# Kernel optimization log

Hardware: AMD Instinct MI355X
Metric: run time of the kernel (lower is better)

Reference implementation:

```python
import jax, jax.numpy as jnp
import numpy as np

N_NODES = 100000
N_EDGES = 1000000
NODE_DIM = 128
LR_VOCAB = 2000
LR_EMBED = 32
HIDDEN = 128
IN_DIM = NODE_DIM * 4 + 1 + LR_EMBED  # 545


def setup_inputs() -> dict:
    key = jax.random.key(0)
    ks = jax.random.split(key, 10)
    z = jax.random.normal(ks[0], (N_NODES, NODE_DIM), dtype=jnp.float32)
    edge_index = jax.random.randint(ks[1], (2, N_EDGES), 0, N_NODES, dtype=jnp.int64)
    # edge_attr7: col 0 = dist (float in [0,1)), col 2 = lr_id (int-valued float in [0, LR_VOCAB))
    ea = jax.random.uniform(ks[2], (N_EDGES, 7), dtype=jnp.float32)
    lr_ids = jax.random.randint(ks[3], (N_EDGES,), 0, LR_VOCAB).astype(jnp.float32)
    edge_attr7 = ea.at[:, 2].set(lr_ids)
    lr_emb = jax.random.normal(ks[4], (LR_VOCAB, LR_EMBED), dtype=jnp.float32) * 0.02
    W1 = jax.random.normal(ks[5], (IN_DIM, HIDDEN), dtype=jnp.float32) * 0.02
    b1 = jnp.zeros((HIDDEN,), dtype=jnp.float32)
    W2 = jax.random.normal(ks[6], (HIDDEN, HIDDEN), dtype=jnp.float32) * 0.02
    b2 = jnp.zeros((HIDDEN,), dtype=jnp.float32)
    W3 = jax.random.normal(ks[7], (HIDDEN, 1), dtype=jnp.float32) * 0.02
    b3 = jnp.zeros((1,), dtype=jnp.float32)
    return {"z": z, "edge_index": edge_index, "edge_attr7": edge_attr7,
            "lr_emb": lr_emb, "W1": W1, "b1": b1, "W2": W2, "b2": b2,
            "W3": W3, "b3": b3}


def reference(z, edge_index, edge_attr7, lr_emb, W1, b1, W2, b2, W3, b3):
    src = edge_index[0]
    dst = edge_index[1]
    zs = z[src]                      # [E, D]
    zd = z[dst]                      # [E, D]
    dist = edge_attr7[:, 0:1]        # [E, 1]
    lr_id = edge_attr7[:, 2].astype(jnp.int32)
    lr_vec = lr_emb[lr_id]           # [E, LR_EMBED]
    x = jnp.concatenate([zs, zd, zs * zd, jnp.abs(zs - zd), dist, lr_vec], axis=1)  # [E, IN_DIM]
    h = jax.nn.relu(x @ W1 + b1)     # dropout is identity at inference
    h = jax.nn.relu(h @ W2 + b2)
    logit = (h @ W3 + b3).reshape(-1)  # [E]
    return logit
```

## Files before the change

kernel.cpp:

```cpp
#include <hip/hip_runtime.h>

#define N_EDGES 1000000
#define HID 128
#define ME 64

typedef unsigned short ushort;
typedef unsigned int uint;
typedef __attribute__((ext_vector_type(8))) short short8;
typedef __attribute__((ext_vector_type(4))) float f32x4;

__device__ __forceinline__ float blo(uint u) { return __builtin_bit_cast(float, u << 16); }
__device__ __forceinline__ float bhi(uint u) { return __builtin_bit_cast(float, u & 0xffff0000u); }
__device__ __forceinline__ ushort f2bfbits(float f) {
  uint u = __builtin_bit_cast(uint, f);
  return (ushort)((u + 0x7fffu + ((u >> 16) & 1u)) >> 16);
}
__device__ __forceinline__ uint cvtpk(float a, float b) {
  uint r;
  asm("v_cvt_pk_bf16_f32 %0, %1, %2" : "=v"(r) : "v"(a), "v"(b));
  return r;
}
__device__ __forceinline__ uint cvtpk_abs(float a, float b) {
  uint r;
  asm("v_cvt_pk_bf16_f32 %0, abs(%1), abs(%2)" : "=v"(r) : "v"(a), "v"(b));
  return r;
}
__device__ __forceinline__ int sidx(int r, int c) {
  return r * 128 + (c ^ ((r & 7) << 3));
}

__global__ void prep_kernel(const float* __restrict__ W1, const float* __restrict__ W2,
                            ushort* __restrict__ W1p, ushort* __restrict__ W2p) {
  const int t = blockIdx.x * blockDim.x + threadIdx.x;
  const int n1 = 18 * 8 * 64 * 8;
  if (t < n1) {
    const int j = t & 7, lane = (t >> 3) & 63, nt = (t >> 9) & 7, kb = t >> 12;
    const int col = nt * 16 + (lane & 15);
    float val = 0.f;
    if (kb < 16) {
      const int k = kb * 32 + (lane >> 4) * 8 + j;
      val = W1[k * HID + col];
    } else {
      const int c = (kb - 16) * 32 + (lane >> 4) * 8 + j;
      const int k = (c == 0) ? 512 : ((c >= 2 && c < 34) ? (511 + c) : -1);
      if (k >= 0) val = W1[k * HID + col];
    }
    W1p[t] = f2bfbits(val);
  } else {
    const int t2 = t - n1;
    if (t2 < 4 * 8 * 64 * 8) {
      const int j = t2 & 7, lane = (t2 >> 3) & 63, nt = (t2 >> 9) & 7, kb = t2 >> 12;
      const int k = kb * 32 + (lane >> 4) * 8 + j;
      const int col = nt * 16 + (lane & 15);
      W2p[t2] = f2bfbits(W2[k * HID + col]);
    }
  }
}

__global__ __launch_bounds__(256, 4)
void edge_mlp(const float* __restrict__ z, const int* __restrict__ ei,
              const float* __restrict__ ea, const float* __restrict__ lre,
              const ushort* __restrict__ W1p, const float* __restrict__ b1,
              const ushort* __restrict__ W2p, const float* __restrict__ b2,
              const float* __restrict__ W3, const float* __restrict__ b3,
              float* __restrict__ out) {
  __shared__ ushort B0[ME * 128];
  __shared__ ushort B1[ME * 128];

  const int tid = threadIdx.x;
  const int lane = tid & 63;
  const int w = tid >> 6;
  const int r15 = lane & 15;
  const int g = lane >> 4;
  const int half = lane >> 5;
  const int li = lane & 31;
  const int row0 = w * 16;
  const int cw = w * 32;
  const int eb = blockIdx.x * ME;

  int sd = 0;
  float auxv = 0.f;
  if (lane < 16)      sd = ei[eb + row0 + lane];
  else if (lane < 32) sd = ei[N_EDGES + eb + row0 + (lane - 16)];
  else if (lane < 48) auxv = ea[(eb + row0 + (lane - 32)) * 7 + 0];
  else                auxv = ea[(eb + row0 + (lane - 48)) * 7 + 2];

  uint2 pr_pk[8], ad_pk[8];
#pragma unroll
  for (int t = 0; t < 8; ++t) {
    const int e = 2 * t + half;
    const int r = row0 + e;
    const int s = __shfl(sd, e);
    const int d = __shfl(sd, 16 + e);
    const float4 a = *(const float4*)(z + s * HID + 4 * li);
    const float4 b = *(const float4*)(z + d * HID + 4 * li);
    uint2 zs, zd;
    zs.x = cvtpk(a.x, a.y); zs.y = cvtpk(a.z, a.w);
    zd.x = cvtpk(b.x, b.y); zd.y = cvtpk(b.z, b.w);
    *(uint2*)&B0[sidx(r, 4 * li)] = zs;
    *(uint2*)&B1[sidx(r, 4 * li)] = zd;
    pr_pk[t].x = cvtpk(a.x * b.x, a.y * b.y);
    pr_pk[t].y = cvtpk(a.z * b.z, a.w * b.w);
    ad_pk[t].x = cvtpk_abs(a.x - b.x, a.y - b.y);
    ad_pk[t].y = cvtpk_abs(a.z - b.z, a.w - b.w);
  }
  __syncthreads();

  f32x4 acc[4][2];
#pragma unroll
  for (int mt = 0; mt < 4; ++mt) {
    acc[mt][0] = (f32x4){0.f, 0.f, 0.f, 0.f};
    acc[mt][1] = (f32x4){0.f, 0.f, 0.f, 0.f};
  }

#define MFMA_CHUNK(BUF, NKK, KB)                                                        \
  _Pragma("unroll")                                                                     \
  for (int kk = 0; kk < (NKK); ++kk) {                                                  \
    const int kbg = (KB) + kk;                                                          \
    short8 bfr0 = *(const short8*)(W1p + (((kbg * 8 + 2 * w) * 64) + lane) * 8);        \
    short8 bfr1 = *(const short8*)(W1p + (((kbg * 8 + 2 * w + 1) * 64) + lane) * 8);    \
    _Pragma("unroll")                                                                   \
    for (int mt = 0; mt < 4; ++mt) {                                                    \
      short8 af = *(const short8*)&BUF[sidx(mt * 16 + r15, ((kbg) & 3) * 32 + g * 8)];  \
      acc[mt][0] = __builtin_amdgcn_mfma_f32_16x16x32_bf16(af, bfr0, acc[mt][0], 0, 0, 0); \
      acc[mt][1] = __builtin_amdgcn_mfma_f32_16x16x32_bf16(af, bfr1, acc[mt][1], 0, 0, 0); \
    }                                                                                   \
  }

  __builtin_amdgcn_s_setprio(1);
  MFMA_CHUNK(B0, 4, 0)
  __builtin_amdgcn_s_setprio(0);
  __syncthreads();

#pragma unroll
  for (int t = 0; t < 8; ++t)
    *(uint2*)&B0[sidx(row0 + 2 * t + half, 4 * li)] = pr_pk[t];
  __builtin_amdgcn_s_setprio(1);
  MFMA_CHUNK(B1, 4, 4)
  __builtin_amdgcn_s_setprio(0);
  __syncthreads();

#pragma unroll
  for (int t = 0; t < 8; ++t)
    *(uint2*)&B1[sidx(row0 + 2 * t + half, 4 * li)] = ad_pk[t];
  __builtin_amdgcn_s_setprio(1);
  MFMA_CHUNK(B0, 4, 8)
  __builtin_amdgcn_s_setprio(0);
  __syncthreads();

  {
    const float dv = __shfl(auxv, 32 + r15);
    if (lane < 16) B0[sidx(row0 + lane, 0)] = f2bfbits(dv);
  }
#pragma unroll
  for (int t = 0; t < 4; ++t) {
    const int e = 4 * t + g;
    const int lrid = (int)__shfl(auxv, 48 + e);
    const float2 lv = *(const float2*)(lre + lrid * 32 + 2 * r15);
    *(uint*)&B0[sidx(row0 + e, 2 + 2 * r15)] = cvtpk(lv.x, lv.y);
  }
  __builtin_amdgcn_s_setprio(1);
  MFMA_CHUNK(B1, 4, 12)
  __builtin_amdgcn_s_setprio(0);
  __syncthreads();

  __builtin_amdgcn_s_setprio(1);
  MFMA_CHUNK(B0, 2, 16)
  __builtin_amdgcn_s_setprio(0);
  {
    const float b1v0 = b1[cw + r15];
    const float b1v1 = b1[cw + 16 + r15];
#pragma unroll
    for (int mt = 0; mt < 4; ++mt)
#pragma unroll
      for (int nt = 0; nt < 2; ++nt)
#pragma unroll
        for (int j = 0; j < 4; ++j) {
          const float h = acc[mt][nt][j] + (nt ? b1v1 : b1v0);
          B1[sidx(mt * 16 + g * 4 + j, cw + nt * 16 + r15)] = f2bfbits(fmaxf(h, 0.f));
        }
  }
  __syncthreads();

#pragma unroll
  for (int mt = 0; mt < 4; ++mt) {
    acc[mt][0] = (f32x4){0.f, 0.f, 0.f, 0.f};
    acc[mt][1] = (f32x4){0.f, 0.f, 0.f, 0.f};
  }
  __builtin_amdgcn_s_setprio(1);
#pragma unroll
  for (int kk = 0; kk < 4; ++kk) {
    short8 bfr0 = *(const short8*)(W2p + (((kk * 8 + 2 * w) * 64) + lane) * 8);
    short8 bfr1 = *(const short8*)(W2p + (((kk * 8 + 2 * w + 1) * 64) + lane) * 8);
#pragma unroll
    for (int mt = 0; mt < 4; ++mt) {
      short8 af = *(const short8*)&B1[sidx(mt * 16 + r15, kk * 32 + g * 8)];
      acc[mt][0] = __builtin_amdgcn_mfma_f32_16x16x32_bf16(af, bfr0, acc[mt][0], 0, 0, 0);
      acc[mt][1] = __builtin_amdgcn_mfma_f32_16x16x32_bf16(af, bfr1, acc[mt][1], 0, 0, 0);
    }
  }
  __builtin_amdgcn_s_setprio(0);
  {
    const float b2v0 = b2[cw + r15];
    const float b2v1 = b2[cw + 16 + r15];
#pragma unroll
    for (int mt = 0; mt < 4; ++mt)
#pragma unroll
      for (int nt = 0; nt < 2; ++nt)
#pragma unroll
        for (int j = 0; j < 4; ++j) {
          const float h = acc[mt][nt][j] + (nt ? b2v1 : b2v0);
          B0[sidx(mt * 16 + g * 4 + j, cw + nt * 16 + r15)] = f2bfbits(fmaxf(h, 0.f));
        }
  }
  __syncthreads();

  {
    const int rr = w * 16 + r15;
    float sum = 0.f;
#pragma unroll
    for (int i = 0; i < 4; ++i) {
      const int c0 = g * 32 + i * 8;
      const uint4 hv = *(const uint4*)&B0[sidx(rr, c0)];
#pragma unroll
      for (int p = 0; p < 4; ++p) {
        const uint u = ((const uint*)&hv)[p];
        const float2 wv = *(const float2*)(W3 + c0 + 2 * p);
        sum += blo(u) * wv.x + bhi(u) * wv.y;
      }
    }
    sum += __shfl_xor(sum, 16);
    sum += __shfl_xor(sum, 32);
    if (lane < 16) out[eb + rr] = sum + b3[0];
  }
}

extern "C" void kernel_launch(void* const* d_in, const int* in_sizes, int n_in,
                              void* d_out, int out_size, void* d_ws, size_t ws_size,
                              hipStream_t stream) {
  const float* z   = (const float*)d_in[0];
  const int*   ei  = (const int*)d_in[1];
  const float* ea  = (const float*)d_in[2];
  const float* lre = (const float*)d_in[3];
  const float* W1  = (const float*)d_in[4];
  const float* b1  = (const float*)d_in[5];
  const float* W2  = (const float*)d_in[6];
  const float* b2  = (const float*)d_in[7];
  const float* W3  = (const float*)d_in[8];
  const float* b3  = (const float*)d_in[9];
  float* out = (float*)d_out;

  ushort* W1p = (ushort*)d_ws;
  ushort* W2p = W1p + 18 * 8 * 64 * 8;

  prep_kernel<<<352, 256, 0, stream>>>(W1, W2, W1p, W2p);
  edge_mlp<<<N_EDGES / ME, 256, 0, stream>>>(z, ei, ea, lre, W1p, b1, W2p, b2, W3, b3, out);
}
```

Baseline: 254.1 us.

## Split edge MLP tile across eight waves with one N-tile per wave

New measurement: 295.8 us. +16.4%, slower.

```diff
diff --git a/kernel.cpp b/kernel.cpp
--- a/kernel.cpp
+++ b/kernel.cpp
@@ -25,6 +25,7 @@
   asm("v_cvt_pk_bf16_f32 %0, abs(%1), abs(%2)" : "=v"(r) : "v"(a), "v"(b));
   return r;
 }
+__device__ __forceinline__ ushort bf1(float a) { return (ushort)cvtpk(a, a); }
 __device__ __forceinline__ int sidx(int r, int c) {
   return r * 128 + (c ^ ((r & 7) << 3));
 }
@@ -57,7 +58,7 @@
   }
 }
 
-__global__ __launch_bounds__(256, 4)
+__global__ __launch_bounds__(512, 6)
 void edge_mlp(const float* __restrict__ z, const int* __restrict__ ei,
               const float* __restrict__ ea, const float* __restrict__ lre,
               const ushort* __restrict__ W1p, const float* __restrict__ b1,
@@ -74,24 +75,24 @@
   const int g = lane >> 4;
   const int half = lane >> 5;
   const int li = lane & 31;
-  const int row0 = w * 16;
-  const int cw = w * 32;
+  const int row0 = w * 8;
+  const int cw = w * 16;
   const int eb = blockIdx.x * ME;
 
   int sd = 0;
   float auxv = 0.f;
-  if (lane < 16)      sd = ei[eb + row0 + lane];
-  else if (lane < 32) sd = ei[N_EDGES + eb + row0 + (lane - 16)];
-  else if (lane < 48) auxv = ea[(eb + row0 + (lane - 32)) * 7 + 0];
-  else                auxv = ea[(eb + row0 + (lane - 48)) * 7 + 2];
-
-  uint2 pr_pk[8], ad_pk[8];
-#pragma unroll
-  for (int t = 0; t < 8; ++t) {
+  if (lane < 8)       sd = ei[eb + row0 + lane];
+  else if (lane < 16) sd = ei[N_EDGES + eb + row0 + (lane - 8)];
+  else if (lane < 24) auxv = ea[(eb + row0 + (lane - 16)) * 7 + 0];
+  else if (lane < 32) auxv = ea[(eb + row0 + (lane - 24)) * 7 + 2];
+
+  uint2 pr_pk[4], ad_pk[4];
+#pragma unroll
+  for (int t = 0; t < 4; ++t) {
     const int e = 2 * t + half;
     const int r = row0 + e;
     const int s = __shfl(sd, e);
-    const int d = __shfl(sd, 16 + e);
+    const int d = __shfl(sd, 8 + e);
     const float4 a = *(const float4*)(z + s * HID + 4 * li);
     const float4 b = *(const float4*)(z + d * HID + 4 * li);
     uint2 zs, zd;
@@ -106,24 +107,19 @@
   }
   __syncthreads();
 
-  f32x4 acc[4][2];
-#pragma unroll
-  for (int mt = 0; mt < 4; ++mt) {
-    acc[mt][0] = (f32x4){0.f, 0.f, 0.f, 0.f};
-    acc[mt][1] = (f32x4){0.f, 0.f, 0.f, 0.f};
-  }
+  f32x4 acc[4];
+#pragma unroll
+  for (int mt = 0; mt < 4; ++mt) acc[mt] = (f32x4){0.f, 0.f, 0.f, 0.f};
 
 #define MFMA_CHUNK(BUF, NKK, KB)                                                        \
   _Pragma("unroll")                                                                     \
   for (int kk = 0; kk < (NKK); ++kk) {                                                  \
     const int kbg = (KB) + kk;                                                          \
-    short8 bfr0 = *(const short8*)(W1p + (((kbg * 8 + 2 * w) * 64) + lane) * 8);        \
-    short8 bfr1 = *(const short8*)(W1p + (((kbg * 8 + 2 * w + 1) * 64) + lane) * 8);    \
+    short8 bfr = *(const short8*)(W1p + (((kbg * 8 + w) * 64) + lane) * 8);             \
     _Pragma("unroll")                                                                   \
     for (int mt = 0; mt < 4; ++mt) {                                                    \
       short8 af = *(const short8*)&BUF[sidx(mt * 16 + r15, ((kbg) & 3) * 32 + g * 8)];  \
-      acc[mt][0] = __builtin_amdgcn_mfma_f32_16x16x32_bf16(af, bfr0, acc[mt][0], 0, 0, 0); \
-      acc[mt][1] = __builtin_amdgcn_mfma_f32_16x16x32_bf16(af, bfr1, acc[mt][1], 0, 0, 0); \
+      acc[mt] = __builtin_amdgcn_mfma_f32_16x16x32_bf16(af, bfr, acc[mt], 0, 0, 0);     \
     }                                                                                   \
   }
 
@@ -133,7 +129,7 @@
   __syncthreads();
 
 #pragma unroll
-  for (int t = 0; t < 8; ++t)
+  for (int t = 0; t < 4; ++t)
     *(uint2*)&B0[sidx(row0 + 2 * t + half, 4 * li)] = pr_pk[t];
   __builtin_amdgcn_s_setprio(1);
   MFMA_CHUNK(B1, 4, 4)
@@ -141,7 +137,7 @@
   __syncthreads();
 
 #pragma unroll
-  for (int t = 0; t < 8; ++t)
+  for (int t = 0; t < 4; ++t)
     *(uint2*)&B1[sidx(row0 + 2 * t + half, 4 * li)] = ad_pk[t];
   __builtin_amdgcn_s_setprio(1);
   MFMA_CHUNK(B0, 4, 8)
@@ -149,13 +145,13 @@
   __syncthreads();
 
   {
-    const float dv = __shfl(auxv, 32 + r15);
-    if (lane < 16) B0[sidx(row0 + lane, 0)] = f2bfbits(dv);
-  }
-#pragma unroll
-  for (int t = 0; t < 4; ++t) {
-    const int e = 4 * t + g;
-    const int lrid = (int)__shfl(auxv, 48 + e);
+    const float dv = __shfl(auxv, 16 + (lane & 7));
+    if (lane < 8) B0[sidx(row0 + lane, 0)] = bf1(dv);
+  }
+#pragma unroll
+  for (int t = 0; t < 2; ++t) {
+    const int e = t * 4 + (lane >> 4);
+    const int lrid = (int)__shfl(auxv, 24 + e);
     const float2 lv = *(const float2*)(lre + lrid * 32 + 2 * r15);
     *(uint*)&B0[sidx(row0 + e, 2 + 2 * r15)] = cvtpk(lv.x, lv.y);
   }
@@ -168,60 +164,50 @@
   MFMA_CHUNK(B0, 2, 16)
   __builtin_amdgcn_s_setprio(0);
   {
-    const float b1v0 = b1[cw + r15];
-    const float b1v1 = b1[cw + 16 + r15];
+    const float b1v = b1[cw + r15];
 #pragma unroll
     for (int mt = 0; mt < 4; ++mt)
 #pragma unroll
-      for (int nt = 0; nt < 2; ++nt)
-#pragma unroll
-        for (int j = 0; j < 4; ++j) {
-          const float h = acc[mt][nt][j] + (nt ? b1v1 : b1v0);
-          B1[sidx(mt * 16 + g * 4 + j, cw + nt * 16 + r15)] = f2bfbits(fmaxf(h, 0.f));
-        }
-  }
-  __syncthreads();
-
-#pragma unroll
-  for (int mt = 0; mt < 4; ++mt) {
-    acc[mt][0] = (f32x4){0.f, 0.f, 0.f, 0.f};
-    acc[mt][1] = (f32x4){0.f, 0.f, 0.f, 0.f};
-  }
+      for (int j = 0; j < 4; ++j) {
+        const float h = fmaxf(acc[mt][j] + b1v, 0.f);
+        B1[sidx(mt * 16 + g * 4 + j, cw + r15)] = bf1(h);
+      }
+  }
+  __syncthreads();
+
+#pragma unroll
+  for (int mt = 0; mt < 4; ++mt) acc[mt] = (f32x4){0.f, 0.f, 0.f, 0.f};
   __builtin_amdgcn_s_setprio(1);
 #pragma unroll
   for (int kk = 0; kk < 4; ++kk) {
-    short8 bfr0 = *(const short8*)(W2p + (((kk * 8 + 2 * w) * 64) + lane) * 8);
-    short8 bfr1 = *(const short8*)(W2p + (((kk * 8 + 2 * w + 1) * 64) + lane) * 8);
+    short8 bfr = *(const short8*)(W2p + (((kk * 8 + w) * 64) + lane) * 8);
 #pragma unroll
     for (int mt = 0; mt < 4; ++mt) {
       short8 af = *(const short8*)&B1[sidx(mt * 16 + r15, kk * 32 + g * 8)];
-      acc[mt][0] = __builtin_amdgcn_mfma_f32_16x16x32_bf16(af, bfr0, acc[mt][0], 0, 0, 0);
-      acc[mt][1] = __builtin_amdgcn_mfma_f32_16x16x32_bf16(af, bfr1, acc[mt][1], 0, 0, 0);
-    }
-  }
-  __builtin_amdgcn_s_setprio(0);
-  {
-    const float b2v0 = b2[cw + r15];
-    const float b2v1 = b2[cw + 16 + r15];
+      acc[mt] = __builtin_amdgcn_mfma_f32_16x16x32_bf16(af, bfr, acc[mt], 0, 0, 0);
+    }
+  }
+  __builtin_amdgcn_s_setprio(0);
+  {
+    const float b2v = b2[cw + r15];
 #pragma unroll
     for (int mt = 0; mt < 4; ++mt)
 #pragma unroll
-      for (int nt = 0; nt < 2; ++nt)
-#pragma unroll
-        for (int j = 0; j < 4; ++j) {
-          const float h = acc[mt][nt][j] + (nt ? b2v1 : b2v0);
-          B0[sidx(mt * 16 + g * 4 + j, cw + nt * 16 + r15)] = f2bfbits(fmaxf(h, 0.f));
-        }
-  }
-  __syncthreads();
-
-  {
-    const int rr = w * 16 + r15;
+      for (int j = 0; j < 4; ++j) {
+        const float h = fmaxf(acc[mt][j] + b2v, 0.f);
+        B0[sidx(mt * 16 + g * 4 + j, cw + r15)] = bf1(h);
+      }
+  }
+  __syncthreads();
+
+  {
+    const int row = w * 8 + (lane >> 3);
+    const int cg = lane & 7;
     float sum = 0.f;
 #pragma unroll
-    for (int i = 0; i < 4; ++i) {
-      const int c0 = g * 32 + i * 8;
-      const uint4 hv = *(const uint4*)&B0[sidx(rr, c0)];
+    for (int i = 0; i < 2; ++i) {
+      const int c0 = cg * 16 + i * 8;
+      const uint4 hv = *(const uint4*)&B0[sidx(row, c0)];
 #pragma unroll
       for (int p = 0; p < 4; ++p) {
         const uint u = ((const uint*)&hv)[p];
@@ -229,9 +215,10 @@
         sum += blo(u) * wv.x + bhi(u) * wv.y;
       }
     }
-    sum += __shfl_xor(sum, 16);
-    sum += __shfl_xor(sum, 32);
-    if (lane < 16) out[eb + rr] = sum + b3[0];
+    sum += __shfl_xor(sum, 1);
+    sum += __shfl_xor(sum, 2);
+    sum += __shfl_xor(sum, 4);
+    if (cg == 0) out[eb + row] = sum + b3[0];
   }
 }
 
@@ -254,5 +241,5 @@
   ushort* W2p = W1p + 18 * 8 * 64 * 8;
 
   prep_kernel<<<352, 256, 0, stream>>>(W1, W2, W1p, W2p);
-  edge_mlp<<<N_EDGES / ME, 256, 0, stream>>>(z, ei, ea, lre, W1p, b1, W2p, b2, W3, b3, out);
-}
+  edge_mlp<<<N_EDGES / ME, 512, 0, stream>>>(z, ei, ea, lre, W1p, b1, W2p, b2, W3, b3, out);
+}
```

## Switch MLP matmuls from 16x16x32 to 32x32x16 bf16 MFMA tiles

Applied to the files above, without the earlier changes.

After: 260.5 us. +2.5%, slower.

```diff
diff --git a/kernel.cpp b/kernel.cpp
--- a/kernel.cpp
+++ b/kernel.cpp
@@ -3,11 +3,12 @@
 #define N_EDGES 1000000
 #define HID 128
 #define ME 64
+#define NK1 35
 
 typedef unsigned short ushort;
 typedef unsigned int uint;
 typedef __attribute__((ext_vector_type(8))) short short8;
-typedef __attribute__((ext_vector_type(4))) float f32x4;
+typedef __attribute__((ext_vector_type(16))) float f32x16;
 
 __device__ __forceinline__ float blo(uint u) { return __builtin_bit_cast(float, u << 16); }
 __device__ __forceinline__ float bhi(uint u) { return __builtin_bit_cast(float, u & 0xffff0000u); }
@@ -25,6 +26,7 @@
   asm("v_cvt_pk_bf16_f32 %0, abs(%1), abs(%2)" : "=v"(r) : "v"(a), "v"(b));
   return r;
 }
+__device__ __forceinline__ ushort bf1(float a) { return (ushort)cvtpk(a, a); }
 __device__ __forceinline__ int sidx(int r, int c) {
   return r * 128 + (c ^ ((r & 7) << 3));
 }
@@ -32,27 +34,25 @@
 __global__ void prep_kernel(const float* __restrict__ W1, const float* __restrict__ W2,
                             ushort* __restrict__ W1p, ushort* __restrict__ W2p) {
   const int t = blockIdx.x * blockDim.x + threadIdx.x;
-  const int n1 = 18 * 8 * 64 * 8;
+  const int n1 = NK1 << 11;
   if (t < n1) {
-    const int j = t & 7, lane = (t >> 3) & 63, nt = (t >> 9) & 7, kb = t >> 12;
-    const int col = nt * 16 + (lane & 15);
+    const int j = t & 7, lane = (t >> 3) & 63, nt = (t >> 9) & 3, ks = t >> 11;
+    const int col = nt * 32 + (lane & 31);
+    const int kk = (lane >> 5) * 8 + j;
     float val = 0.f;
-    if (kb < 16) {
-      const int k = kb * 32 + (lane >> 4) * 8 + j;
-      val = W1[k * HID + col];
+    if (ks < 32) {
+      val = W1[(ks * 16 + kk) * HID + col];
     } else {
-      const int c = (kb - 16) * 32 + (lane >> 4) * 8 + j;
+      const int c = (ks - 32) * 16 + kk;
       const int k = (c == 0) ? 512 : ((c >= 2 && c < 34) ? (511 + c) : -1);
       if (k >= 0) val = W1[k * HID + col];
     }
     W1p[t] = f2bfbits(val);
   } else {
     const int t2 = t - n1;
-    if (t2 < 4 * 8 * 64 * 8) {
-      const int j = t2 & 7, lane = (t2 >> 3) & 63, nt = (t2 >> 9) & 7, kb = t2 >> 12;
-      const int k = kb * 32 + (lane >> 4) * 8 + j;
-      const int col = nt * 16 + (lane & 15);
-      W2p[t2] = f2bfbits(W2[k * HID + col]);
+    if (t2 < (8 << 11)) {
+      const int j = t2 & 7, lane = (t2 >> 3) & 63, nt = (t2 >> 9) & 3, ks = t2 >> 11;
+      W2p[t2] = f2bfbits(W2[(ks * 16 + (lane >> 5) * 8 + j) * HID + nt * 32 + (lane & 31)]);
     }
   }
 }
@@ -74,6 +74,7 @@
   const int g = lane >> 4;
   const int half = lane >> 5;
   const int li = lane & 31;
+  const int hi = lane >> 5;
   const int row0 = w * 16;
   const int cw = w * 32;
   const int eb = blockIdx.x * ME;
@@ -106,29 +107,26 @@
   }
   __syncthreads();
 
-  f32x4 acc[4][2];
-#pragma unroll
-  for (int mt = 0; mt < 4; ++mt) {
-    acc[mt][0] = (f32x4){0.f, 0.f, 0.f, 0.f};
-    acc[mt][1] = (f32x4){0.f, 0.f, 0.f, 0.f};
-  }
-
-#define MFMA_CHUNK(BUF, NKK, KB)                                                        \
+  f32x16 acc[2];
+#pragma unroll
+  for (int mt = 0; mt < 2; ++mt)
+#pragma unroll
+    for (int rg = 0; rg < 16; ++rg) acc[mt][rg] = 0.f;
+
+#define MFMA_KS(BUF, WP, NKS, KS0)                                                      \
   _Pragma("unroll")                                                                     \
-  for (int kk = 0; kk < (NKK); ++kk) {                                                  \
-    const int kbg = (KB) + kk;                                                          \
-    short8 bfr0 = *(const short8*)(W1p + (((kbg * 8 + 2 * w) * 64) + lane) * 8);        \
-    short8 bfr1 = *(const short8*)(W1p + (((kbg * 8 + 2 * w + 1) * 64) + lane) * 8);    \
+  for (int ks = 0; ks < (NKS); ++ks) {                                                  \
+    const int ksg = (KS0) + ks;                                                         \
+    short8 bfr = *(const short8*)((WP) + (((ksg * 4 + w) * 64) + lane) * 8);            \
     _Pragma("unroll")                                                                   \
-    for (int mt = 0; mt < 4; ++mt) {                                                    \
-      short8 af = *(const short8*)&BUF[sidx(mt * 16 + r15, ((kbg) & 3) * 32 + g * 8)];  \
-      acc[mt][0] = __builtin_amdgcn_mfma_f32_16x16x32_bf16(af, bfr0, acc[mt][0], 0, 0, 0); \
-      acc[mt][1] = __builtin_amdgcn_mfma_f32_16x16x32_bf16(af, bfr1, acc[mt][1], 0, 0, 0); \
+    for (int mt = 0; mt < 2; ++mt) {                                                    \
+      short8 af = *(const short8*)&BUF[sidx(mt * 32 + li, ((ksg & 7) * 16) + hi * 8)];  \
+      acc[mt] = __builtin_amdgcn_mfma_f32_32x32x16_bf16(af, bfr, acc[mt], 0, 0, 0);     \
     }                                                                                   \
   }
 
   __builtin_amdgcn_s_setprio(1);
-  MFMA_CHUNK(B0, 4, 0)
+  MFMA_KS(B0, W1p, 8, 0)
   __builtin_amdgcn_s_setprio(0);
   __syncthreads();
 
@@ -136,7 +134,7 @@
   for (int t = 0; t < 8; ++t)
     *(uint2*)&B0[sidx(row0 + 2 * t + half, 4 * li)] = pr_pk[t];
   __builtin_amdgcn_s_setprio(1);
-  MFMA_CHUNK(B1, 4, 4)
+  MFMA_KS(B1, W1p, 8, 8)
   __builtin_amdgcn_s_setprio(0);
   __syncthreads();
 
@@ -144,13 +142,13 @@
   for (int t = 0; t < 8; ++t)
     *(uint2*)&B1[sidx(row0 + 2 * t + half, 4 * li)] = ad_pk[t];
   __builtin_amdgcn_s_setprio(1);
-  MFMA_CHUNK(B0, 4, 8)
+  MFMA_KS(B0, W1p, 8, 16)
   __builtin_amdgcn_s_setprio(0);
   __syncthreads();
 
   {
     const float dv = __shfl(auxv, 32 + r15);
-    if (lane < 16) B0[sidx(row0 + lane, 0)] = f2bfbits(dv);
+    if (lane < 16) B0[sidx(row0 + lane, 0)] = bf1(dv);
   }
 #pragma unroll
   for (int t = 0; t < 4; ++t) {
@@ -160,58 +158,43 @@
     *(uint*)&B0[sidx(row0 + e, 2 + 2 * r15)] = cvtpk(lv.x, lv.y);
   }
   __builtin_amdgcn_s_setprio(1);
-  MFMA_CHUNK(B1, 4, 12)
-  __builtin_amdgcn_s_setprio(0);
-  __syncthreads();
-
-  __builtin_amdgcn_s_setprio(1);
-  MFMA_CHUNK(B0, 2, 16)
-  __builtin_amdgcn_s_setprio(0);
-  {
-    const float b1v0 = b1[cw + r15];
-    const float b1v1 = b1[cw + 16 + r15];
-#pragma unroll
-    for (int mt = 0; mt < 4; ++mt)
-#pragma unroll
-      for (int nt = 0; nt < 2; ++nt)
-#pragma unroll
-        for (int j = 0; j < 4; ++j) {
-          const float h = acc[mt][nt][j] + (nt ? b1v1 : b1v0);
-          B1[sidx(mt * 16 + g * 4 + j, cw + nt * 16 + r15)] = f2bfbits(fmaxf(h, 0.f));
-        }
-  }
-  __syncthreads();
-
-#pragma unroll
-  for (int mt = 0; mt < 4; ++mt) {
-    acc[mt][0] = (f32x4){0.f, 0.f, 0.f, 0.f};
-    acc[mt][1] = (f32x4){0.f, 0.f, 0.f, 0.f};
-  }
-  __builtin_amdgcn_s_setprio(1);
-#pragma unroll
-  for (int kk = 0; kk < 4; ++kk) {
-    short8 bfr0 = *(const short8*)(W2p + (((kk * 8 + 2 * w) * 64) + lane) * 8);
-    short8 bfr1 = *(const short8*)(W2p + (((kk * 8 + 2 * w + 1) * 64) + lane) * 8);
-#pragma unroll
-    for (int mt = 0; mt < 4; ++mt) {
-      short8 af = *(const short8*)&B1[sidx(mt * 16 + r15, kk * 32 + g * 8)];
-      acc[mt][0] = __builtin_amdgcn_mfma_f32_16x16x32_bf16(af, bfr0, acc[mt][0], 0, 0, 0);
-      acc[mt][1] = __builtin_amdgcn_mfma_f32_16x16x32_bf16(af, bfr1, acc[mt][1], 0, 0, 0);
-    }
-  }
-  __builtin_amdgcn_s_setprio(0);
-  {
-    const float b2v0 = b2[cw + r15];
-    const float b2v1 = b2[cw + 16 + r15];
-#pragma unroll
-    for (int mt = 0; mt < 4; ++mt)
-#pragma unroll
-      for (int nt = 0; nt < 2; ++nt)
-#pragma unroll
-        for (int j = 0; j < 4; ++j) {
-          const float h = acc[mt][nt][j] + (nt ? b2v1 : b2v0);
-          B0[sidx(mt * 16 + g * 4 + j, cw + nt * 16 + r15)] = f2bfbits(fmaxf(h, 0.f));
-        }
+  MFMA_KS(B1, W1p, 8, 24)
+  __builtin_amdgcn_s_setprio(0);
+  __syncthreads();
+
+  __builtin_amdgcn_s_setprio(1);
+  MFMA_KS(B0, W1p, 3, 32)
+  __builtin_amdgcn_s_setprio(0);
+  {
+    const float b1v = b1[cw + li];
+#pragma unroll
+    for (int mt = 0; mt < 2; ++mt)
+#pragma unroll
+      for (int rg = 0; rg < 16; ++rg) {
+        const int row = mt * 32 + (rg & 3) + 8 * (rg >> 2) + 4 * hi;
+        const float h = fmaxf(acc[mt][rg] + b1v, 0.f);
+        B1[sidx(row, cw + li)] = bf1(h);
+      }
+  }
+  __syncthreads();
+
+#pragma unroll
+  for (int mt = 0; mt < 2; ++mt)
+#pragma unroll
+    for (int rg = 0; rg < 16; ++rg) acc[mt][rg] = 0.f;
+  __builtin_amdgcn_s_setprio(1);
+  MFMA_KS(B1, W2p, 8, 0)
+  __builtin_amdgcn_s_setprio(0);
+  {
+    const float b2v = b2[cw + li];
+#pragma unroll
+    for (int mt = 0; mt < 2; ++mt)
+#pragma unroll
+      for (int rg = 0; rg < 16; ++rg) {
+        const int row = mt * 32 + (rg & 3) + 8 * (rg >> 2) + 4 * hi;
+        const float h = fmaxf(acc[mt][rg] + b2v, 0.f);
+        B0[sidx(row, cw + li)] = bf1(h);
+      }
   }
   __syncthreads();
 
@@ -251,8 +234,8 @@
   float* out = (float*)d_out;
 
   ushort* W1p = (ushort*)d_ws;
-  ushort* W2p = W1p + 18 * 8 * 64 * 8;
-
-  prep_kernel<<<352, 256, 0, stream>>>(W1, W2, W1p, W2p);
+  ushort* W2p = W1p + (NK1 << 11);
+
+  prep_kernel<<<344, 256, 0, stream>>>(W1, W2, W1p, W2p);
   edge_mlp<<<N_EDGES / ME, 256, 0, stream>>>(z, ei, ea, lre, W1p, b1, W2p, b2, W3, b3, out);
 }
```
